# Performance work log

Measured on AMD Instinct MI355X. Metric: run time of the kernel, lower is better.

Reference implementation:

```python
import jax, jax.numpy as jnp
import numpy as np

NUM_HEADS = 12

def setup_inputs() -> dict:
    key = jax.random.key(0)
    ks = jax.random.split(key, 6)
    B, N, C = 16, 1024, 768
    H, d = NUM_HEADS, C // NUM_HEADS
    return {
        "x": jax.random.normal(ks[0], (B, N, C), dtype=jnp.float32),
        "W_qkv": jax.random.normal(ks[1], (C, 3 * C), dtype=jnp.float32) * 0.02,
        "b_qkv": jax.random.normal(ks[2], (3 * C,), dtype=jnp.float32) * 0.02,
        "zeta": jnp.ones((1, 1, H, 1, d), dtype=jnp.float32),
        "W_proj": jax.random.normal(ks[3], (C, C), dtype=jnp.float32) * 0.02,
        "b_proj": jax.random.normal(ks[4], (C,), dtype=jnp.float32) * 0.02,
        "mask": jnp.zeros((B, N), dtype=bool),
    }

def reference(x, W_qkv, b_qkv, zeta, W_proj, b_proj, mask):
    B, N, C = x.shape
    H = NUM_HEADS
    d = C // H
    scale = d ** -0.5
    # qkv: (B,N,3C) -> (B,N,3,H,d) -> (3,B,H,N,d), gated by zeta (1,1,H,1,d)
    qkv = (x @ W_qkv + b_qkv).reshape(B, N, 3, H, d).transpose(2, 0, 3, 1, 4)
    qkv = qkv * zeta
    q, k, v = qkv[0], qkv[1], qkv[2]
    attn = jnp.einsum("bhnd,bhmd->bhnm", q, k) * scale
    # mask (B,N) over keys -> (B,1,1,N)
    attn = jnp.where(mask[:, None, None, :], -jnp.inf, attn)
    attn = jax.nn.softmax(attn, axis=-1)
    out = jnp.einsum("bhnm,bhmd->bhnd", attn, v)          # (B,H,N,d)
    out = out.transpose(0, 2, 1, 3).reshape(B, N, C)
    return out @ W_proj + b_proj
```

## Files before the change

kernel.cpp:

```cpp
#include <hip/hip_runtime.h>
#include <hip/hip_bf16.h>

typedef unsigned short ushort_t;
typedef __bf16 bf16_t;
typedef bf16_t bf16x8 __attribute__((ext_vector_type(8)));
typedef float floatx4 __attribute__((ext_vector_type(4)));
typedef ushort_t ushortx8 __attribute__((ext_vector_type(8)));

struct alignas(8) us4 { ushort_t x, y, z, w; };

__device__ __forceinline__ ushort_t f2bf(float f) {
  union { float f; unsigned int u; } v; v.f = f;
  unsigned int u = v.u;
  return (ushort_t)((u + 0x7fffu + ((u >> 16) & 1u)) >> 16);
}

__device__ __forceinline__ unsigned int pk_bf16(float a, float b) {
  __hip_bfloat162 h = __float22bfloat162_rn(float2{a, b});
  union { __hip_bfloat162 h; unsigned int u; } v; v.h = h;
  return v.u;
}

__device__ __forceinline__ void async16(const void* g, void* l) {
  __builtin_amdgcn_global_load_lds(
      (const __attribute__((address_space(1))) unsigned int*)g,
      (__attribute__((address_space(3))) unsigned int*)l, 16, 0, 0);
}

#define LOG2E 1.44269504088896340736f


__global__ __launch_bounds__(256) void k_prep(const float* __restrict__ x,
                                              ushort_t* __restrict__ xb,
                                              const float* __restrict__ Wq,
                                              ushort_t* __restrict__ WqT,
                                              const float* __restrict__ Wp,
                                              ushort_t* __restrict__ WpT) {
  __shared__ float tile[32][33];
  const int bid = blockIdx.x, t = threadIdx.x;
  if (bid < 6144) {
    size_t i = ((size_t)bid * 256 + t) * 8;
    float4 a = *(const float4*)(x + i);
    float4 b = *(const float4*)(x + i + 4);
    ushortx8 o;
    o[0] = f2bf(a.x); o[1] = f2bf(a.y); o[2] = f2bf(a.z); o[3] = f2bf(a.w);
    o[4] = f2bf(b.x); o[5] = f2bf(b.y); o[6] = f2bf(b.z); o[7] = f2bf(b.w);
    *(ushortx8*)(xb + i) = o;
    return;
  }
  const float* in; ushort_t* out; int C, c0, r0;
  if (bid < 7872) {
    int b2 = bid - 6144;
    in = Wq; out = WqT; C = 2304;
    c0 = (b2 % 72) * 32; r0 = (b2 / 72) * 32;
  } else {
    int b3 = bid - 7872;
    in = Wp; out = WpT; C = 768;
    c0 = (b3 % 24) * 32; r0 = (b3 / 24) * 32;
  }
  const int tx = t & 31, ty = t >> 5;
#pragma unroll
  for (int i = 0; i < 32; i += 8)
    tile[ty + i][tx] = in[(size_t)(r0 + ty + i) * C + c0 + tx];
  __syncthreads();
#pragma unroll
  for (int i = 0; i < 32; i += 8)
    out[(size_t)(c0 + ty + i) * 768 + r0 + tx] = f2bf(tile[tx][ty + i]);
}


template <bool SWAP>
__device__ __forceinline__ void gemm_pipe3(const ushort_t* __restrict__ A,
                                           const ushort_t* __restrict__ Bt,
                                           int m0, int n0,
                                           ushort_t* sA, ushort_t* sB,
                                           floatx4 acc[4][4]) {
  const int t = threadIdx.x;
  const int lane = t & 63;
  const int lr = lane & 15, qd = lane >> 4;
  const int w = t >> 6;
  const int wr = w >> 1, wc = w & 1;
  const int swz = ((t & 3) ^ ((t >> 3) & 3)) * 8;
  const ushort_t* gA = A + (size_t)(m0 + (t >> 2)) * 768 + swz;
  const ushort_t* gB = Bt + (size_t)(n0 + (t >> 2)) * 768 + swz;
  char* lA = (char*)sA + t * 16;
  char* lB = (char*)sB + t * 16;
  const int rsz = (qd ^ ((lr >> 1) & 3)) * 16;
#define ISSUE(kk, buf)                                    \
  do {                                                    \
    const int k0_ = (kk) * 32, b_ = (buf) * 8192;         \
    async16(gA + k0_, lA + b_);                           \
    async16(gA + k0_ + 64 * 768, lA + b_ + 4096);         \
    async16(gB + k0_, lB + b_);                           \
    async16(gB + k0_ + 64 * 768, lB + b_ + 4096);         \
  } while (0)
  ISSUE(0, 0);
  ISSUE(1, 1);
  asm volatile("s_waitcnt vmcnt(4)" ::: "memory");
  asm volatile("s_barrier" ::: "memory");
#pragma unroll
  for (int k = 0; k < 24; ++k) {
    if (k + 2 < 24) ISSUE(k + 2, (k + 2) % 3);
    const char* cA = (const char*)sA + (k % 3) * 8192;
    const char* cB = (const char*)sB + (k % 3) * 8192;
    bf16x8 af[4], bfr[4];
#pragma unroll
    for (int i = 0; i < 4; ++i)
      af[i] = *(const bf16x8*)(cA + (wr * 64 + i * 16 + lr) * 64 + rsz);
#pragma unroll
    for (int j = 0; j < 4; ++j)
      bfr[j] = *(const bf16x8*)(cB + (wc * 64 + j * 16 + lr) * 64 + rsz);
#pragma unroll
    for (int i = 0; i < 4; ++i)
#pragma unroll
      for (int j = 0; j < 4; ++j) {
        if constexpr (SWAP)
          acc[i][j] = __builtin_amdgcn_mfma_f32_16x16x32_bf16(bfr[j], af[i], acc[i][j], 0, 0, 0);
        else
          acc[i][j] = __builtin_amdgcn_mfma_f32_16x16x32_bf16(af[i], bfr[j], acc[i][j], 0, 0, 0);
      }
    if (k < 22)
      asm volatile("s_waitcnt vmcnt(4)" ::: "memory");
    else if (k == 22)
      asm volatile("s_waitcnt vmcnt(0)" ::: "memory");
    if (k < 23) asm volatile("s_barrier" ::: "memory");
  }
#undef ISSUE
}


__global__ __launch_bounds__(256, 3) void k_qkv(const ushort_t* __restrict__ xb,
                                                const ushort_t* __restrict__ WqT,
                                                const float* __restrict__ bqkv,
                                                const float* __restrict__ zeta,
                                                ushort_t* __restrict__ qb,
                                                ushort_t* __restrict__ kb,
                                                ushort_t* __restrict__ vtb) {
  __shared__ alignas(16) ushort_t sA[3 * 4096];
  __shared__ alignas(16) ushort_t sB[3 * 4096];
  floatx4 acc[4][4] = {};
  const int lin = blockIdx.x;
  const int xcd = lin & 7, idx = lin >> 3;
  const int m0 = (xcd * 16 + (idx & 15)) * 128;
  const int n0 = (idx >> 4) * 128;
  const int tq = n0 / 768;
  const int t = threadIdx.x, lane = t & 63, w = t >> 6;
  const int wr = w >> 1, wc = w & 1, lr = lane & 15, qd = lane >> 4;
  if (tq < 2) {
    gemm_pipe3<true>(xb, WqT, m0, n0, sA, sB, acc);
    ushort_t* dst = (tq == 0) ? qb : kb;
    const float sc = (tq == 0) ? 0.125f * LOG2E : 1.0f;
#pragma unroll
    for (int j = 0; j < 4; ++j) {
      int n = n0 + wc * 64 + j * 16 + qd * 4;
      int nc = n - tq * 768;
      int h = nc >> 6, dim = n & 63;
      float4 b4 = *(const float4*)&bqkv[n];
      float4 z4 = *(const float4*)&zeta[nc];
      float g0 = z4.x * sc, g1 = z4.y * sc, g2 = z4.z * sc, g3 = z4.w * sc;
#pragma unroll
      for (int i = 0; i < 4; ++i) {
        int m = m0 + wr * 64 + i * 16 + lr;
        int b = m >> 10, seq = m & 1023;
        us4 pk;
        pk.x = f2bf((acc[i][j][0] + b4.x) * g0);
        pk.y = f2bf((acc[i][j][1] + b4.y) * g1);
        pk.z = f2bf((acc[i][j][2] + b4.z) * g2);
        pk.w = f2bf((acc[i][j][3] + b4.w) * g3);
        *(us4*)&dst[(((size_t)b * 12 + h) * 1024 + seq) * 64 + dim] = pk;
      }
    }
  } else {
    gemm_pipe3<false>(xb, WqT, m0, n0, sA, sB, acc);
#pragma unroll
    for (int j = 0; j < 4; ++j) {
      int n = n0 + wc * 64 + j * 16 + lr;
      int nc = n - 2 * 768;
      int h = nc >> 6, dim = n & 63;
      float bias = bqkv[n];
      float zv = zeta[nc];
#pragma unroll
      for (int i = 0; i < 4; ++i) {
        int mbase = m0 + wr * 64 + i * 16 + qd * 4;
        int b = mbase >> 10, seq = mbase & 1023;
        us4 pk;
        pk.x = f2bf((acc[i][j][0] + bias) * zv);
        pk.y = f2bf((acc[i][j][1] + bias) * zv);
        pk.z = f2bf((acc[i][j][2] + bias) * zv);
        pk.w = f2bf((acc[i][j][3] + bias) * zv);
        *(us4*)&vtb[(((size_t)b * 12 + h) * 64 + dim) * 1024 + seq] = pk;
      }
    }
  }
}


__global__ __launch_bounds__(256, 3) void k_attn(const ushort_t* __restrict__ qg,
                                                 const ushort_t* __restrict__ kg,
                                                 const ushort_t* __restrict__ vg,
                                                 const unsigned char* __restrict__ mask,
                                                 ushort_t* __restrict__ ob) {
  __shared__ alignas(16) char smem[53248];
  float* maskadd = (float*)(smem + 49152);
  const int t = threadIdx.x, lane = t & 63, w = t >> 6;
  const int lr = lane & 15, qd = lane >> 4;
  const int lin = blockIdx.x;
  const int bh = (lin & 7) + 8 * (lin >> 6);
  const int qt = (lin >> 3) & 7;
  const int b = bh / 12, h = bh % 12;
  const int qrow0 = qt * 128 + w * 32;
  const ushort_t* qp = qg + (size_t)bh * 65536;
  const ushort_t* kp = kg + (size_t)bh * 65536;
  const ushort_t* vp = vg + (size_t)bh * 65536;
  const unsigned char* mp = mask + b * 1024;

  bf16x8 qf[2][2];
#pragma unroll
  for (int ns = 0; ns < 2; ++ns)
#pragma unroll
    for (int kk = 0; kk < 2; ++kk)
      qf[ns][kk] = *(const bf16x8*)(qp + (size_t)(qrow0 + ns * 16 + lr) * 64 + kk * 32 + qd * 8);

  floatx4 o[4][2] = {};
  float lst[2] = {0.f, 0.f};
  char* sPw = smem + 32768 + w * 4096;

  {
    uchar4 mv = *(const uchar4*)(mp + t * 4);
    float4 f;
    f.x = mv.x ? -1e30f : 0.0f;
    f.y = mv.y ? -1e30f : 0.0f;
    f.z = mv.z ? -1e30f : 0.0f;
    f.w = mv.w ? -1e30f : 0.0f;
    *(float4*)&maskadd[t * 4] = f;
  }

#define STAGE_K(kt_, st_)                                                 \
  do {                                                                    \
    const ushort_t* kpt_ = kp + (kt_) * 4096;                             \
    _Pragma("unroll")                                                     \
    for (int it = 0; it < 2; ++it) {                                      \
      int p = it * 256 + t;                                               \
      int r = p >> 3, cs = (p & 7) ^ (r & 7);                             \
      async16(kpt_ + r * 64 + cs * 8, smem + (st_) * 16384 + p * 16);     \
    }                                                                     \
  } while (0)
#define STAGE_V(kt_, st_)                                                 \
  do {                                                                    \
    const ushort_t* vpt_ = vp + (kt_) * 64;                               \
    _Pragma("unroll")                                                     \
    for (int it = 0; it < 2; ++it) {                                      \
      int p = it * 256 + t;                                               \
      int r = p >> 3, cs = (p & 7) ^ (r & 7);                             \
      async16(vpt_ + (size_t)r * 1024 + cs * 8,                           \
              smem + (st_) * 16384 + 8192 + p * 16);                      \
    }                                                                     \
  } while (0)

  STAGE_K(0, 0);
  STAGE_V(0, 0);
  __syncthreads();

#pragma unroll 2
  for (int kt = 0; kt < 16; ++kt) {
    const int st = kt & 1;
    if (kt + 1 < 16) {
      STAGE_K(kt + 1, st ^ 1);
      STAGE_V(kt + 1, st ^ 1);
    }
    const char* sK = smem + st * 16384;
    const char* sV = smem + st * 16384 + 8192;

    floatx4 s[4][2] = {};
    __builtin_amdgcn_s_setprio(1);
#pragma unroll
    for (int kk = 0; kk < 2; ++kk) {
#pragma unroll
      for (int ms = 0; ms < 4; ++ms) {
        bf16x8 ak = *(const bf16x8*)(sK + (ms * 16 + lr) * 128 +
                                     ((kk * 4 + qd) ^ (lr & 7)) * 16);
#pragma unroll
        for (int ns = 0; ns < 2; ++ns)
          s[ms][ns] = __builtin_amdgcn_mfma_f32_16x16x32_bf16(ak, qf[ns][kk], s[ms][ns], 0, 0, 0);
      }
    }
    __builtin_amdgcn_s_setprio(0);

#pragma unroll
    for (int ms = 0; ms < 4; ++ms) {
      float4 mk = *(const float4*)&maskadd[kt * 64 + ms * 16 + qd * 4];
#pragma unroll
      for (int ns = 0; ns < 2; ++ns) {
        float p0 = __builtin_amdgcn_exp2f(s[ms][ns][0] + mk.x);
        float p1 = __builtin_amdgcn_exp2f(s[ms][ns][1] + mk.y);
        float p2 = __builtin_amdgcn_exp2f(s[ms][ns][2] + mk.z);
        float p3 = __builtin_amdgcn_exp2f(s[ms][ns][3] + mk.w);
        lst[ns] += (p0 + p1) + (p2 + p3);
        uint2 pk;
        pk.x = pk_bf16(p0, p1);
        pk.y = pk_bf16(p2, p3);
        *(uint2*)(sPw + (ns * 16 + lr) * 128 +
                  ((ms * 2 + (qd >> 1)) ^ (lr & 7)) * 16 + (qd & 1) * 8) = pk;
      }
    }
    asm volatile("s_waitcnt lgkmcnt(0)" ::: "memory");
    __builtin_amdgcn_sched_barrier(0);

    if (kt + 1 < 16)
      asm volatile("s_waitcnt vmcnt(4)" ::: "memory");
    else
      asm volatile("s_waitcnt vmcnt(0)" ::: "memory");
    asm volatile("s_barrier" ::: "memory");

    __builtin_amdgcn_s_setprio(1);
#pragma unroll
    for (int kk = 0; kk < 2; ++kk) {
      bf16x8 pb[2];
#pragma unroll
      for (int ns = 0; ns < 2; ++ns)
        pb[ns] = *(const bf16x8*)(sPw + (ns * 16 + lr) * 128 +
                                  ((kk * 4 + qd) ^ (lr & 7)) * 16);
#pragma unroll
      for (int ds = 0; ds < 4; ++ds) {
        bf16x8 av = *(const bf16x8*)(sV + (ds * 16 + lr) * 128 +
                                     ((kk * 4 + qd) ^ (lr & 7)) * 16);
#pragma unroll
        for (int ns = 0; ns < 2; ++ns)
          o[ds][ns] = __builtin_amdgcn_mfma_f32_16x16x32_bf16(av, pb[ns], o[ds][ns], 0, 0, 0);
      }
    }
    __builtin_amdgcn_s_setprio(0);

    if (kt + 1 < 16) {
      asm volatile("s_waitcnt vmcnt(2)" ::: "memory");
      asm volatile("s_barrier" ::: "memory");
    }
  }
#undef STAGE_K
#undef STAGE_V

#pragma unroll
  for (int ns = 0; ns < 2; ++ns) {
    lst[ns] += __shfl_xor(lst[ns], 16);
    lst[ns] += __shfl_xor(lst[ns], 32);
  }
#pragma unroll
  for (int ns = 0; ns < 2; ++ns) {
    float rl = 1.0f / lst[ns];
    size_t row = (size_t)(b * 1024 + qrow0 + ns * 16 + lr) * 768 + h * 64;
#pragma unroll
    for (int ds = 0; ds < 4; ++ds) {
      uint2 ov;
      ov.x = pk_bf16(o[ds][ns][0] * rl, o[ds][ns][1] * rl);
      ov.y = pk_bf16(o[ds][ns][2] * rl, o[ds][ns][3] * rl);
      *(uint2*)&ob[row + ds * 16 + qd * 4] = ov;
    }
  }
}


__global__ __launch_bounds__(256, 3) void k_proj(const ushort_t* __restrict__ ob,
                                                 const ushort_t* __restrict__ WpT,
                                                 const float* __restrict__ bproj,
                                                 float* __restrict__ out) {
  __shared__ alignas(16) ushort_t sA[3 * 4096];
  __shared__ alignas(16) ushort_t sB[3 * 4096];
  floatx4 acc[4][4] = {};
  const int lin = blockIdx.x;
  const int xcd = lin & 7, idx = lin >> 3;
  const int m0 = (xcd * 16 + (idx & 15)) * 128;
  const int n0 = (idx >> 4) * 128;
  gemm_pipe3<true>(ob, WpT, m0, n0, sA, sB, acc);
  const int t = threadIdx.x, lane = t & 63, w = t >> 6;
  const int wr = w >> 1, wc = w & 1, lr = lane & 15, qd = lane >> 4;
#pragma unroll
  for (int j = 0; j < 4; ++j) {
    int n = n0 + wc * 64 + j * 16 + qd * 4;
    float4 b4 = *(const float4*)&bproj[n];
#pragma unroll
    for (int i = 0; i < 4; ++i) {
      int m = m0 + wr * 64 + i * 16 + lr;
      float4 o;
      o.x = acc[i][j][0] + b4.x;
      o.y = acc[i][j][1] + b4.y;
      o.z = acc[i][j][2] + b4.z;
      o.w = acc[i][j][3] + b4.w;
      *(float4*)&out[(size_t)m * 768 + n] = o;
    }
  }
}


extern "C" void kernel_launch(void* const* d_in, const int* in_sizes, int n_in,
                              void* d_out, int out_size, void* d_ws, size_t ws_size,
                              hipStream_t stream) {
  const float* x = (const float*)d_in[0];
  const float* bqkv = (const float*)d_in[2];
  const float* zeta = (const float*)d_in[3];
  const float* bproj = (const float*)d_in[5];
  const unsigned char* mask = (const unsigned char*)d_in[6];
  float* out = (float*)d_out;
  char* ws = (char*)d_ws;
  ushort_t* xb  = (ushort_t*)(ws);
  ushort_t* WqT = (ushort_t*)(ws + 25165824);
  ushort_t* WpT = (ushort_t*)(ws + 28704768);
  ushort_t* qb  = (ushort_t*)(ws + 29884416);
  ushort_t* kb  = (ushort_t*)(ws + 55050240);
  ushort_t* vtb = (ushort_t*)(ws + 80216064);
  ushort_t* ob  = xb;

  k_prep<<<dim3(8448), dim3(256), 0, stream>>>(x, xb, (const float*)d_in[1], WqT,
                                               (const float*)d_in[4], WpT);
  k_qkv<<<dim3(2304), dim3(256), 0, stream>>>(xb, WqT, bqkv, zeta, qb, kb, vtb);
  k_attn<<<dim3(1536), dim3(256), 0, stream>>>(qb, kb, vtb, mask, ob);
  k_proj<<<dim3(768), dim3(256), 0, stream>>>(ob, WpT, bproj, out);
}
```

Measured before the change: 290.2 us.

## Enlarge QKV GEMM tile to 256x256 with 512-thread blocks and double buffering

Replaces the QKV projection GEMM's 128x128 tile, 256-thread, triple-buffered pipeline with a 256x256 tile computed by 8 waves (2x4), each holding 8x4 MFMA accumulators, and a double-buffered LDS pipeline that waits on vmcnt(0) every k step. The grid shrinks from 2304 to 576 blocks. The larger tile raises arithmetic intensity and cuts redundant global loads of x and W. The trade-offs are higher register pressure, fewer blocks (576 against the CU count) and a shallower prefetch with a full wait each iteration. It also fixes the epilogue dim index to use nc&63, which gives the same value since 768 is a multiple of 64.

Result: slower. 303.0 us (+4.4%).

```diff
diff --git a/kernel.cpp b/kernel.cpp
--- a/kernel.cpp
+++ b/kernel.cpp
@@ -66,6 +66,130 @@
 #pragma unroll
   for (int i = 0; i < 32; i += 8)
     out[(size_t)(c0 + ty + i) * 768 + r0 + tx] = f2bf(tile[tx][ty + i]);
+}
+
+
+template <bool SWAP>
+__device__ __forceinline__ void gemm256(const ushort_t* __restrict__ A,
+                                        const ushort_t* __restrict__ Bt,
+                                        int m0, int n0,
+                                        ushort_t* sA, ushort_t* sB,
+                                        floatx4 acc[8][4]) {
+  const int t = threadIdx.x;
+  const int lane = t & 63;
+  const int lr = lane & 15, qd = lane >> 4;
+  const int w = t >> 6;
+  const int wr = w >> 2, wc = w & 3;
+  const int swz = ((t & 3) ^ ((t >> 3) & 3)) * 8;
+  const ushort_t* gA = A + (size_t)(m0 + (t >> 2)) * 768 + swz;
+  const ushort_t* gB = Bt + (size_t)(n0 + (t >> 2)) * 768 + swz;
+  char* lA = (char*)sA + t * 16;
+  char* lB = (char*)sB + t * 16;
+  const int rsz = (qd ^ ((lr >> 1) & 3)) * 16;
+#define ISSUE(kk, buf)                                    \
+  do {                                                    \
+    const int k0_ = (kk) * 32, b_ = (buf) * 16384;        \
+    async16(gA + k0_, lA + b_);                           \
+    async16(gA + k0_ + 128 * 768, lA + b_ + 8192);        \
+    async16(gB + k0_, lB + b_);                           \
+    async16(gB + k0_ + 128 * 768, lB + b_ + 8192);        \
+  } while (0)
+  ISSUE(0, 0);
+  asm volatile("s_waitcnt vmcnt(0)" ::: "memory");
+  asm volatile("s_barrier" ::: "memory");
+#pragma unroll
+  for (int k = 0; k < 24; ++k) {
+    if (k + 1 < 24) ISSUE(k + 1, (k + 1) & 1);
+    const char* cA = (const char*)sA + (k & 1) * 16384;
+    const char* cB = (const char*)sB + (k & 1) * 16384;
+    bf16x8 af[8], bfr[4];
+#pragma unroll
+    for (int i = 0; i < 8; ++i)
+      af[i] = *(const bf16x8*)(cA + (wr * 128 + i * 16 + lr) * 64 + rsz);
+#pragma unroll
+    for (int j = 0; j < 4; ++j)
+      bfr[j] = *(const bf16x8*)(cB + (wc * 64 + j * 16 + lr) * 64 + rsz);
+#pragma unroll
+    for (int i = 0; i < 8; ++i)
+#pragma unroll
+      for (int j = 0; j < 4; ++j) {
+        if constexpr (SWAP)
+          acc[i][j] = __builtin_amdgcn_mfma_f32_16x16x32_bf16(bfr[j], af[i], acc[i][j], 0, 0, 0);
+        else
+          acc[i][j] = __builtin_amdgcn_mfma_f32_16x16x32_bf16(af[i], bfr[j], acc[i][j], 0, 0, 0);
+      }
+    if (k + 1 < 24) {
+      asm volatile("s_waitcnt vmcnt(0)" ::: "memory");
+      asm volatile("s_barrier" ::: "memory");
+    }
+  }
+#undef ISSUE
+}
+
+
+__global__ __launch_bounds__(512, 2) void k_qkv(const ushort_t* __restrict__ xb,
+                                                const ushort_t* __restrict__ WqT,
+                                                const float* __restrict__ bqkv,
+                                                const float* __restrict__ zeta,
+                                                ushort_t* __restrict__ qb,
+                                                ushort_t* __restrict__ kb,
+                                                ushort_t* __restrict__ vtb) {
+  __shared__ alignas(16) ushort_t sA[2 * 8192];
+  __shared__ alignas(16) ushort_t sB[2 * 8192];
+  floatx4 acc[8][4] = {};
+  const int lin = blockIdx.x;
+  const int xcd = lin & 7, idx = lin >> 3;
+  const int m0 = (xcd * 8 + (idx & 7)) * 256;
+  const int n0 = (idx >> 3) * 256;
+  const int tq = n0 / 768;
+  const int t = threadIdx.x, lane = t & 63, w = t >> 6;
+  const int wr = w >> 2, wc = w & 3, lr = lane & 15, qd = lane >> 4;
+  if (tq < 2) {
+    gemm256<true>(xb, WqT, m0, n0, sA, sB, acc);
+    ushort_t* dst = (tq == 0) ? qb : kb;
+    const float sc = (tq == 0) ? 0.125f * LOG2E : 1.0f;
+#pragma unroll
+    for (int j = 0; j < 4; ++j) {
+      int n = n0 + wc * 64 + j * 16 + qd * 4;
+      int nc = n - tq * 768;
+      int h = nc >> 6, dim = nc & 63;
+      float4 b4 = *(const float4*)&bqkv[n];
+      float4 z4 = *(const float4*)&zeta[nc];
+      float g0 = z4.x * sc, g1 = z4.y * sc, g2 = z4.z * sc, g3 = z4.w * sc;
+#pragma unroll
+      for (int i = 0; i < 8; ++i) {
+        int m = m0 + wr * 128 + i * 16 + lr;
+        int b = m >> 10, seq = m & 1023;
+        us4 pk;
+        pk.x = f2bf((acc[i][j][0] + b4.x) * g0);
+        pk.y = f2bf((acc[i][j][1] + b4.y) * g1);
+        pk.z = f2bf((acc[i][j][2] + b4.z) * g2);
+        pk.w = f2bf((acc[i][j][3] + b4.w) * g3);
+        *(us4*)&dst[(((size_t)b * 12 + h) * 1024 + seq) * 64 + dim] = pk;
+      }
+    }
+  } else {
+    gemm256<false>(xb, WqT, m0, n0, sA, sB, acc);
+#pragma unroll
+    for (int j = 0; j < 4; ++j) {
+      int n = n0 + wc * 64 + j * 16 + lr;
+      int nc = n - 2 * 768;
+      int h = nc >> 6, dim = nc & 63;
+      float bias = bqkv[n];
+      float zv = zeta[nc];
+#pragma unroll
+      for (int i = 0; i < 8; ++i) {
+        int mbase = m0 + wr * 128 + i * 16 + qd * 4;
+        int b = mbase >> 10, seq = mbase & 1023;
+        us4 pk;
+        pk.x = f2bf((acc[i][j][0] + bias) * zv);
+        pk.y = f2bf((acc[i][j][1] + bias) * zv);
+        pk.z = f2bf((acc[i][j][2] + bias) * zv);
+        pk.w = f2bf((acc[i][j][3] + bias) * zv);
+        *(us4*)&vtb[(((size_t)b * 12 + h) * 64 + dim) * 1024 + seq] = pk;
+      }
+    }
+  }
 }
 
 
@@ -129,72 +253,6 @@
 }
 
 
-__global__ __launch_bounds__(256, 3) void k_qkv(const ushort_t* __restrict__ xb,
-                                                const ushort_t* __restrict__ WqT,
-                                                const float* __restrict__ bqkv,
-                                                const float* __restrict__ zeta,
-                                                ushort_t* __restrict__ qb,
-                                                ushort_t* __restrict__ kb,
-                                                ushort_t* __restrict__ vtb) {
-  __shared__ alignas(16) ushort_t sA[3 * 4096];
-  __shared__ alignas(16) ushort_t sB[3 * 4096];
-  floatx4 acc[4][4] = {};
-  const int lin = blockIdx.x;
-  const int xcd = lin & 7, idx = lin >> 3;
-  const int m0 = (xcd * 16 + (idx & 15)) * 128;
-  const int n0 = (idx >> 4) * 128;
-  const int tq = n0 / 768;
-  const int t = threadIdx.x, lane = t & 63, w = t >> 6;
-  const int wr = w >> 1, wc = w & 1, lr = lane & 15, qd = lane >> 4;
-  if (tq < 2) {
-    gemm_pipe3<true>(xb, WqT, m0, n0, sA, sB, acc);
-    ushort_t* dst = (tq == 0) ? qb : kb;
-    const float sc = (tq == 0) ? 0.125f * LOG2E : 1.0f;
-#pragma unroll
-    for (int j = 0; j < 4; ++j) {
-      int n = n0 + wc * 64 + j * 16 + qd * 4;
-      int nc = n - tq * 768;
-      int h = nc >> 6, dim = n & 63;
-      float4 b4 = *(const float4*)&bqkv[n];
-      float4 z4 = *(const float4*)&zeta[nc];
-      float g0 = z4.x * sc, g1 = z4.y * sc, g2 = z4.z * sc, g3 = z4.w * sc;
-#pragma unroll
-      for (int i = 0; i < 4; ++i) {
-        int m = m0 + wr * 64 + i * 16 + lr;
-        int b = m >> 10, seq = m & 1023;
-        us4 pk;
-        pk.x = f2bf((acc[i][j][0] + b4.x) * g0);
-        pk.y = f2bf((acc[i][j][1] + b4.y) * g1);
-        pk.z = f2bf((acc[i][j][2] + b4.z) * g2);
-        pk.w = f2bf((acc[i][j][3] + b4.w) * g3);
-        *(us4*)&dst[(((size_t)b * 12 + h) * 1024 + seq) * 64 + dim] = pk;
-      }
-    }
-  } else {
-    gemm_pipe3<false>(xb, WqT, m0, n0, sA, sB, acc);
-#pragma unroll
-    for (int j = 0; j < 4; ++j) {
-      int n = n0 + wc * 64 + j * 16 + lr;
-      int nc = n - 2 * 768;
-      int h = nc >> 6, dim = n & 63;
-      float bias = bqkv[n];
-      float zv = zeta[nc];
-#pragma unroll
-      for (int i = 0; i < 4; ++i) {
-        int mbase = m0 + wr * 64 + i * 16 + qd * 4;
-        int b = mbase >> 10, seq = mbase & 1023;
-        us4 pk;
-        pk.x = f2bf((acc[i][j][0] + bias) * zv);
-        pk.y = f2bf((acc[i][j][1] + bias) * zv);
-        pk.z = f2bf((acc[i][j][2] + bias) * zv);
-        pk.w = f2bf((acc[i][j][3] + bias) * zv);
-        *(us4*)&vtb[(((size_t)b * 12 + h) * 64 + dim) * 1024 + seq] = pk;
-      }
-    }
-  }
-}
-
-
 __global__ __launch_bounds__(256, 3) void k_attn(const ushort_t* __restrict__ qg,
                                                  const ushort_t* __restrict__ kg,
                                                  const ushort_t* __restrict__ vg,
@@ -411,7 +469,7 @@
 
   k_prep<<<dim3(8448), dim3(256), 0, stream>>>(x, xb, (const float*)d_in[1], WqT,
                                                (const float*)d_in[4], WpT);
-  k_qkv<<<dim3(2304), dim3(256), 0, stream>>>(xb, WqT, bqkv, zeta, qb, kb, vtb);
+  k_qkv<<<dim3(576), dim3(512), 0, stream>>>(xb, WqT, bqkv, zeta, qb, kb, vtb);
   k_attn<<<dim3(1536), dim3(256), 0, stream>>>(qb, kb, vtb, mask, ob);
   k_proj<<<dim3(768), dim3(256), 0, stream>>>(ob, WpT, bproj, out);
 }
```
